# Kernel tuning notes

Hardware: AMD Instinct MI355X
Metric: run time of the kernel (lower is better)

Reference implementation:

```python
import jax, jax.numpy as jnp
import numpy as np

D_MODEL = 1024
N_HEADS = 16
D_HEAD = D_MODEL // N_HEADS
B, S = 4, 2048
NEG_INF = float('-inf')


def setup_inputs() -> dict:
    key = jax.random.key(0)
    ks = jax.random.split(key, 12)
    sc = 1.0 / np.sqrt(D_MODEL)
    inp = {
        'query': jax.random.normal(ks[0], (B, S, D_MODEL), jnp.float32),
        'key': jax.random.normal(ks[1], (B, S, D_MODEL), jnp.float32),
        'value': jax.random.normal(ks[2], (B, S, D_MODEL), jnp.float32),
        'mask': jnp.ones((B, S), jnp.int32),
        'W_q': jax.random.normal(ks[3], (D_MODEL, D_MODEL), jnp.float32) * sc,
        'b_q': jax.random.normal(ks[4], (D_MODEL,), jnp.float32) * sc,
        'W_k': jax.random.normal(ks[5], (D_MODEL, D_MODEL), jnp.float32) * sc,
        'b_k': jax.random.normal(ks[6], (D_MODEL,), jnp.float32) * sc,
        'W_v': jax.random.normal(ks[7], (D_MODEL, D_MODEL), jnp.float32) * sc,
        'b_v': jax.random.normal(ks[8], (D_MODEL,), jnp.float32) * sc,
        'W_o': jax.random.normal(ks[9], (D_MODEL, D_MODEL), jnp.float32) * sc,
        'b_o': jax.random.normal(ks[10], (D_MODEL,), jnp.float32) * sc,
    }
    return inp


def reference(query, key, value, mask, W_q, b_q, W_k, b_k, W_v, b_v, W_o, b_o):
    b, s, d = query.shape
    # QKV projections, split heads: [B,S,D] -> [B,H,S,Dh]
    def proj(x, W, bias):
        y = x @ W + bias
        return y.reshape(b, s, N_HEADS, D_HEAD).transpose(0, 2, 1, 3)
    q = proj(query, W_q, b_q)
    k = proj(key, W_k, b_k)
    v = proj(value, W_v, b_v)
    # NOTE: original scales by d_head**2 (not sqrt) — kept faithful.
    e = jnp.einsum('bhqd,bhkd->bhqk', q, k) / (D_HEAD ** 2)
    # key padding mask: [B,S] -> additive [B,1,1,S]
    pad = jnp.where(mask == 0, NEG_INF, 0.0).astype(e.dtype)[:, None, None, :]
    e = e + pad
    # causal mask: additive lower-triangular
    causal = jnp.where(jnp.tril(jnp.ones((s, s), bool)), 0.0, NEG_INF).astype(e.dtype)
    e = e + causal[None, None, :, :]
    a = jax.nn.softmax(e, axis=-1)
    c = jnp.einsum('bhqk,bhkd->bhqd', a, v)  # [B,H,S,Dh]
    c = c.transpose(0, 2, 1, 3).reshape(b, s, d)
    return c @ W_o + b_o
```

## Files before the change

### kernel.cpp

```cpp
#include <hip/hip_runtime.h>

typedef __bf16 bf16;
typedef unsigned int u32;
typedef float f32x4 __attribute__((ext_vector_type(4)));
typedef __bf16 bf16x4 __attribute__((ext_vector_type(4)));
typedef __bf16 bf16x8 __attribute__((ext_vector_type(8)));

#define MFMA(a, b, c) __builtin_amdgcn_mfma_f32_16x16x32_bf16((a), (b), (c), 0, 0, 0)

static constexpr int Bc = 4;
static constexpr int Sc = 2048;
static constexpr int Hc = 16;
static constexpr int DHc = 64;
static constexpr int Dc = 1024;
static constexpr int Mc = Bc * Sc;

__device__ __forceinline__ void load_lds16(const bf16* gp, bf16* lp) {
    __builtin_amdgcn_global_load_lds(
        reinterpret_cast<const __attribute__((address_space(1))) u32*>(
            reinterpret_cast<uintptr_t>(gp)),
        reinterpret_cast<__attribute__((address_space(3))) u32*>(
            static_cast<u32>(reinterpret_cast<uintptr_t>(lp))),
        16, 0, 0);
}

__global__ void fill_diag(float* out, int n) {
    int i = blockIdx.x * 256 + threadIdx.x;
    if (i < n) out[i] = 1000.0f;
}

__global__ __launch_bounds__(256) void cvt_bf16(const float* __restrict__ in,
                                                bf16* __restrict__ out, int n) {
    int i = (blockIdx.x * 256 + threadIdx.x) * 8;
    if (i < n) {
        f32x4 a = *(const f32x4*)&in[i];
        f32x4 b = *(const f32x4*)&in[i + 4];
        bf16x8 v;
#pragma unroll
        for (int j = 0; j < 4; ++j) { v[j] = (bf16)a[j]; v[j + 4] = (bf16)b[j]; }
        *(bf16x8*)&out[i] = v;
    }
}

__global__ __launch_bounds__(256) void transpose4(
    const float* __restrict__ A0, const float* __restrict__ A1,
    const float* __restrict__ A2, const float* __restrict__ A3,
    bf16* __restrict__ O0, bf16* __restrict__ O1,
    bf16* __restrict__ O2, bf16* __restrict__ O3) {
    __shared__ bf16 t[32][33];
    const float* in = blockIdx.z == 0 ? A0 : blockIdx.z == 1 ? A1
                    : blockIdx.z == 2 ? A2 : A3;
    bf16* out = blockIdx.z == 0 ? O0 : blockIdx.z == 1 ? O1
              : blockIdx.z == 2 ? O2 : O3;
    int x = blockIdx.x * 32 + threadIdx.x;
#pragma unroll
    for (int j = 0; j < 32; j += 8) {
        int y = blockIdx.y * 32 + threadIdx.y + j;
        t[threadIdx.y + j][threadIdx.x] = (bf16)in[y * 1024 + x];
    }
    __syncthreads();
    int x2 = blockIdx.y * 32 + threadIdx.x;
#pragma unroll
    for (int j = 0; j < 32; j += 8) {
        int y2 = blockIdx.x * 32 + threadIdx.y + j;
        out[y2 * 1024 + x2] = t[threadIdx.x][threadIdx.y + j];
    }
}

template <int MODE, typename TOUT>
__global__ __launch_bounds__(256) void gemm_bt(const bf16* __restrict__ A,
                                               const bf16* __restrict__ Wt,
                                               const float* __restrict__ bias,
                                               TOUT* __restrict__ out,
                                               int M, int N, int K) {
    __shared__ alignas(16) bf16 As[3][128 * 32];
    __shared__ alignas(16) bf16 Bs[3][128 * 32];
    const int tid = threadIdx.x;
    const int wave = tid >> 6, lane = tid & 63;
    const int quad = lane >> 4, l16 = lane & 15;
    const int wr = (wave >> 1) * 64, wc = (wave & 1) * 64;
    const int id = blockIdx.y * 8 + blockIdx.x;
    const int sw = (id & 7) * 64 + (id >> 3);
    const int row0 = (sw >> 3) * 128, col0 = (sw & 7) * 128;

    const int sr = wave * 32 + (lane >> 2);
    const int sk = (lane & 3) * 8;
    const bf16* gA = &A[(size_t)(row0 + sr) * K + sk];
    const bf16* gB = &Wt[(size_t)(col0 + sr) * K + sk];
    const int wo = wave * 32 * 32;

#define GSTAGE(BUF, KOFF)                                                   \
    do {                                                                    \
        load_lds16(gA + (KOFF), &As[BUF][wo]);                              \
        load_lds16(gA + (KOFF) + 16 * K, &As[BUF][wo + 16 * 32]);           \
        load_lds16(gB + (KOFF), &Bs[BUF][wo]);                              \
        load_lds16(gB + (KOFF) + 16 * K, &Bs[BUF][wo + 16 * 32]);           \
    } while (0)

    f32x4 acc[4][4];
#pragma unroll
    for (int mi = 0; mi < 4; ++mi)
#pragma unroll
        for (int ni = 0; ni < 4; ++ni)
            acc[mi][ni] = (f32x4){0.f, 0.f, 0.f, 0.f};

    const int nk = K / 32;
    GSTAGE(0, 0);
    GSTAGE(1, 32);
    asm volatile("s_waitcnt vmcnt(4)" ::: "memory");
    __builtin_amdgcn_s_barrier();
    __builtin_amdgcn_sched_barrier(0);

    int cur = 0, nxt = 2;
#pragma unroll 1
    for (int i = 0; i < nk; ++i) {
        if (i + 2 < nk) GSTAGE(nxt, (i + 2) * 32);

        bf16x8 af[4], bf_[4];
#pragma unroll
        for (int mi = 0; mi < 4; ++mi)
            af[mi] = *(const bf16x8*)&As[cur][(wr + mi * 16 + l16) * 32 + quad * 8];
#pragma unroll
        for (int ni = 0; ni < 4; ++ni)
            bf_[ni] = *(const bf16x8*)&Bs[cur][(wc + ni * 16 + l16) * 32 + quad * 8];
#pragma unroll
        for (int mi = 0; mi < 4; ++mi)
#pragma unroll
            for (int ni = 0; ni < 4; ++ni)
                acc[mi][ni] = MFMA(af[mi], bf_[ni], acc[mi][ni]);

        if (i + 2 < nk) asm volatile("s_waitcnt vmcnt(4)" ::: "memory");
        else            asm volatile("s_waitcnt vmcnt(0)" ::: "memory");
        __builtin_amdgcn_s_barrier();
        __builtin_amdgcn_sched_barrier(0);
        cur = (cur == 2) ? 0 : cur + 1;
        nxt = (nxt == 2) ? 0 : nxt + 1;
    }
#undef GSTAGE

#pragma unroll
    for (int mi = 0; mi < 4; ++mi) {
#pragma unroll
        for (int ni = 0; ni < 4; ++ni) {
            int col = col0 + wc + ni * 16 + l16;
            float bv = bias[col];
#pragma unroll
            for (int r = 0; r < 4; ++r) {
                int row = row0 + wr + mi * 16 + quad * 4 + r;
                float v = acc[mi][ni][r] + bv;
                size_t off;
                if (MODE == 0) {
                    off = (size_t)row * N + col;
                } else {
                    int b = row >> 11, s = row & (Sc - 1);
                    int h = col >> 6, dh = col & (DHc - 1);
                    if (MODE == 1)
                        off = (((size_t)(b * Hc + h) * Sc + s) << 6) + dh;
                    else
                        off = (((size_t)(b * Hc + h) * DHc + dh) << 11) + s;
                }
                out[off] = (TOUT)v;
            }
        }
    }
}

static constexpr int LPP = 72;
static constexpr float CEXP = 1.4426950408889634f / 4096.0f;

__global__ __launch_bounds__(256, 2) void attn_fwd(const bf16* __restrict__ Q,
                                                   const bf16* __restrict__ K,
                                                   const bf16* __restrict__ Vt,
                                                   const int* __restrict__ mask,
                                                   bf16* __restrict__ Ctx) {
    __shared__ alignas(16) bf16 Ks[2][64 * 64];
    __shared__ alignas(16) bf16 Vs[2][64 * 64];
    __shared__ alignas(16) bf16 Ps[4][32 * LPP];
    __shared__ alignas(16) float msk_all[Sc];

    const int tid = threadIdx.x;
    const int wave = tid >> 6, lane = tid & 63;
    const int quad = lane >> 4, l16 = lane & 15;
    const int id = blockIdx.y * 8 + blockIdx.x;
    const int sw = (id & 7) * 64 + (id >> 3);
    const int bh = sw >> 3, p = sw & 7;
    const int b = bh >> 4, h = bh & 15;

    {
        const int i = tid * 8;
        int4 m0 = *(const int4*)&mask[b * Sc + i];
        int4 m1 = *(const int4*)&mask[b * Sc + i + 4];
        f32x4 f0 = {m0.x ? 0.f : -1e30f, m0.y ? 0.f : -1e30f,
                    m0.z ? 0.f : -1e30f, m0.w ? 0.f : -1e30f};
        f32x4 f1 = {m1.x ? 0.f : -1e30f, m1.y ? 0.f : -1e30f,
                    m1.z ? 0.f : -1e30f, m1.w ? 0.f : -1e30f};
        *(f32x4*)&msk_all[i] = f0;
        *(f32x4*)&msk_all[i + 4] = f1;
    }

    const int swz = ((lane & 7) ^ (lane >> 3)) << 4;
    const int rA = wave * 16 + (lane >> 3);
    const char* gK0 = (const char*)K + (size_t)bh * Sc * (DHc * 2)
                    + (size_t)rA * 128 + swz;
    const char* gV0 = (const char*)Vt + (size_t)bh * DHc * (Sc * 2)
                    + (size_t)rA * (Sc * 2) + swz;
    bf16* lK0 = &Ks[0][(wave * 16) * 64];
    bf16* lV0 = &Vs[0][(wave * 16) * 64];

    const int m7 = l16 & 7;
    const int gsw0 = ((0 + quad) ^ m7) * 8;
    const int gsw1 = ((4 + quad) ^ m7) * 8;

#define STAGE(BUF, KB)                                                        \
    do {                                                                      \
        load_lds16((const bf16*)(gK0 + (size_t)(KB) * 128),                   \
                   lK0 + (BUF) * (64 * 64));                                  \
        load_lds16((const bf16*)(gK0 + (size_t)(KB) * 128 + 1024),            \
                   lK0 + (BUF) * (64 * 64) + 8 * 64);                         \
        load_lds16((const bf16*)(gV0 + (size_t)(KB) * 2),                     \
                   lV0 + (BUF) * (64 * 64));                                  \
        load_lds16((const bf16*)(gV0 + (size_t)(KB) * 2 + 8 * 4096),          \
                   lV0 + (BUF) * (64 * 64) + 8 * 64);                         \
    } while (0)

#pragma unroll 1
    for (int pass = 0; pass < 2; ++pass) {
        const int qt = pass ? p : 15 - p;
        const int qr0 = qt * 128 + wave * 32;
        const int qmax = qr0 + 31;

        bf16x8 bq[2][2];
#pragma unroll
        for (int mt = 0; mt < 2; ++mt) {
            const size_t qoff = ((size_t)bh * Sc + qr0 + mt * 16 + l16) * DHc;
            bq[mt][0] = *(const bf16x8*)&Q[qoff + quad * 8];
            bq[mt][1] = *(const bf16x8*)&Q[qoff + 32 + quad * 8];
        }

        f32x4 accO[2][4];
#pragma unroll
        for (int mt = 0; mt < 2; ++mt)
#pragma unroll
            for (int oi = 0; oi < 4; ++oi) accO[mt][oi] = (f32x4){0.f, 0.f, 0.f, 0.f};
        float l_part[2] = {0.f, 0.f};

        const int nkt = 2 * qt + 2;
        STAGE(0, 0);
        __syncthreads();
        int cur = 0;
#pragma unroll 1
        for (int kt = 0; kt < nkt; ++kt) {
            const int kb = kt * 64;
            if (kt + 1 < nkt) STAGE(cur ^ 1, kb + 64);
            if (kb <= qmax) {
                const bf16* Kb_ = &Ks[cur][0];
                const bf16* Vb_ = &Vs[cur][0];

                f32x4 st[2][4];
                __builtin_amdgcn_s_setprio(1);
#pragma unroll
                for (int kti = 0; kti < 4; ++kti) {
                    bf16x8 ak0 = *(const bf16x8*)&Kb_[(kti * 16 + l16) * 64 + gsw0];
                    bf16x8 ak1 = *(const bf16x8*)&Kb_[(kti * 16 + l16) * 64 + gsw1];
#pragma unroll
                    for (int mt = 0; mt < 2; ++mt) {
                        f32x4 z = {0.f, 0.f, 0.f, 0.f};
                        z = MFMA(ak0, bq[mt][0], z);
                        z = MFMA(ak1, bq[mt][1], z);
                        st[mt][kti] = z;
                    }
                }
                __builtin_amdgcn_s_setprio(0);

#define SM_TILE(DIAG)                                                          \
                _Pragma("unroll")                                              \
                for (int mt = 0; mt < 2; ++mt) {                               \
                    _Pragma("unroll")                                          \
                    for (int kti = 0; kti < 4; ++kti) {                        \
                        const f32x4 mkv =                                      \
                            *(const f32x4*)&msk_all[kb + kti * 16 + quad * 4]; \
                        const int cbase =                                      \
                            kb + kti * 16 + quad * 4 - (qr0 + mt * 16);        \
                        bf16x4 pv;                                             \
                        _Pragma("unroll")                                      \
                        for (int r = 0; r < 4; ++r) {                          \
                            float s = st[mt][kti][r] * CEXP + mkv[r];          \
                            if (DIAG) s = (cbase + r > l16) ? -1e30f : s;      \
                            float p_ = __builtin_amdgcn_exp2f(s);              \
                            l_part[mt] += p_;                                  \
                            pv[r] = (bf16)p_;                                  \
                        }                                                      \
                        *(bf16x4*)&Ps[wave][(mt * 16 + l16) * LPP +            \
                                            kti * 16 + quad * 4] = pv;         \
                    }                                                          \
                }
                if (kb + 63 > qr0) { SM_TILE(1) } else { SM_TILE(0) }
#undef SM_TILE

                __builtin_amdgcn_s_setprio(1);
#pragma unroll
                for (int kk = 0; kk < 2; ++kk) {
                    bf16x8 ap0 = *(const bf16x8*)&Ps[wave][(l16) * LPP + kk * 32 + quad * 8];
                    bf16x8 ap1 = *(const bf16x8*)&Ps[wave][(16 + l16) * LPP + kk * 32 + quad * 8];
                    const int vg = kk ? gsw1 : gsw0;
#pragma unroll
                    for (int oi = 0; oi < 4; ++oi) {
                        bf16x8 bv = *(const bf16x8*)&Vb_[(oi * 16 + l16) * 64 + vg];
                        accO[0][oi] = MFMA(ap0, bv, accO[0][oi]);
                        accO[1][oi] = MFMA(ap1, bv, accO[1][oi]);
                    }
                }
                __builtin_amdgcn_s_setprio(0);
            }
            asm volatile("s_waitcnt vmcnt(0)" ::: "memory");
            __builtin_amdgcn_s_barrier();
            __builtin_amdgcn_sched_barrier(0);
            cur ^= 1;
        }

        float lvi[2][4];
#pragma unroll
        for (int mt = 0; mt < 2; ++mt) {
            float l = l_part[mt];
            l += __shfl_xor(l, 16);
            l += __shfl_xor(l, 32);
#pragma unroll
            for (int r = 0; r < 4; ++r)
                lvi[mt][r] = __builtin_amdgcn_rcpf(__shfl(l, quad * 4 + r));
        }
#pragma unroll
        for (int mt = 0; mt < 2; ++mt)
#pragma unroll
            for (int oi = 0; oi < 4; ++oi)
#pragma unroll
                for (int r = 0; r < 4; ++r) {
                    int s = qr0 + mt * 16 + quad * 4 + r;
                    int dh = oi * 16 + l16;
                    float v = accO[mt][oi][r] * lvi[mt][r];
                    Ctx[((size_t)b * Sc + s) * Dc + h * DHc + dh] = (bf16)v;
                }
    }
#undef STAGE
}

extern "C" void kernel_launch(void* const* d_in, const int* in_sizes, int n_in,
                              void* d_out, int out_size, void* d_ws, size_t ws_size,
                              hipStream_t stream) {
    const float* query = (const float*)d_in[0];
    const float* key_i = (const float*)d_in[1];
    const float* value = (const float*)d_in[2];
    const int* mask    = (const int*)d_in[3];
    const float* W_q = (const float*)d_in[4];
    const float* b_q = (const float*)d_in[5];
    const float* W_k = (const float*)d_in[6];
    const float* b_k = (const float*)d_in[7];
    const float* W_v = (const float*)d_in[8];
    const float* b_v = (const float*)d_in[9];
    const float* W_o = (const float*)d_in[10];
    const float* b_o = (const float*)d_in[11];
    float* out = (float*)d_out;

    const size_t MB = 1024 * 1024;
    const size_t NEED = 72 * MB;
    if (ws_size < NEED) {
        fill_diag<<<(out_size + 255) / 256, 256, 0, stream>>>(out, out_size);
        return;
    }

    char* ws = (char*)d_ws;
    bf16* WtQ = (bf16*)(ws + 0 * MB);
    bf16* WtK = (bf16*)(ws + 2 * MB);
    bf16* WtV = (bf16*)(ws + 4 * MB);
    bf16* WtO = (bf16*)(ws + 6 * MB);
    bf16* Xin = (bf16*)(ws + 8 * MB);
    bf16* Ctx = (bf16*)(ws + 8 * MB);
    bf16* Qb  = (bf16*)(ws + 24 * MB);
    bf16* Kb  = (bf16*)(ws + 40 * MB);
    bf16* Vtb = (bf16*)(ws + 56 * MB);

    transpose4<<<dim3(32, 32, 4), dim3(32, 8), 0, stream>>>(
        W_q, W_k, W_v, W_o, WtQ, WtK, WtV, WtO);

    const int ncv = Mc * Dc;
    dim3 gg(Dc / 128, Mc / 128);

    cvt_bf16<<<ncv / (256 * 8), 256, 0, stream>>>(query, Xin, ncv);
    gemm_bt<1, bf16><<<gg, 256, 0, stream>>>(Xin, WtQ, b_q, Qb, Mc, Dc, Dc);
    cvt_bf16<<<ncv / (256 * 8), 256, 0, stream>>>(key_i, Xin, ncv);
    gemm_bt<1, bf16><<<gg, 256, 0, stream>>>(Xin, WtK, b_k, Kb, Mc, Dc, Dc);
    cvt_bf16<<<ncv / (256 * 8), 256, 0, stream>>>(value, Xin, ncv);
    gemm_bt<2, bf16><<<gg, 256, 0, stream>>>(Xin, WtV, b_v, Vtb, Mc, Dc, Dc);

    attn_fwd<<<dim3(8, Bc * Hc), 256, 0, stream>>>(Qb, Kb, Vtb, mask, Ctx);

    gemm_bt<0, float><<<gg, 256, 0, stream>>>(Ctx, WtO, b_o, out, Mc, Dc, Dc);
}
```

Measured before the change: 319.6 us.

## Fuse fp32-to-bf16 input conversion into a batched QKV projection GEMM

Removes the three separate cvt_bf16 passes and three projection GEMM launches. A single z-batched gemm_qkv kernel loads fp32 activations straight into LDS with a swizzled layout and converts them to bf16 in registers before the MFMA. This drops the write and re-read of the bf16 copy of each input and cuts the launch count. In exchange, the A tile in LDS is twice as large (fp32), the kernel uses double buffering with a full vmcnt(0) wait each iteration instead of the triple-buffered pipeline, and each fragment load pays extra conversion ALU work.

```diff
diff --git a/kernel.cpp b/kernel.cpp
--- a/kernel.cpp
+++ b/kernel.cpp
@@ -15,7 +15,7 @@
 static constexpr int Dc = 1024;
 static constexpr int Mc = Bc * Sc;
 
-__device__ __forceinline__ void load_lds16(const bf16* gp, bf16* lp) {
+__device__ __forceinline__ void load_lds16(const void* gp, void* lp) {
     __builtin_amdgcn_global_load_lds(
         reinterpret_cast<const __attribute__((address_space(1))) u32*>(
             reinterpret_cast<uintptr_t>(gp)),
@@ -27,19 +27,6 @@
 __global__ void fill_diag(float* out, int n) {
     int i = blockIdx.x * 256 + threadIdx.x;
     if (i < n) out[i] = 1000.0f;
-}
-
-__global__ __launch_bounds__(256) void cvt_bf16(const float* __restrict__ in,
-                                                bf16* __restrict__ out, int n) {
-    int i = (blockIdx.x * 256 + threadIdx.x) * 8;
-    if (i < n) {
-        f32x4 a = *(const f32x4*)&in[i];
-        f32x4 b = *(const f32x4*)&in[i + 4];
-        bf16x8 v;
-#pragma unroll
-        for (int j = 0; j < 4; ++j) { v[j] = (bf16)a[j]; v[j + 4] = (bf16)b[j]; }
-        *(bf16x8*)&out[i] = v;
-    }
 }
 
 __global__ __launch_bounds__(256) void transpose4(
@@ -67,11 +54,123 @@
     }
 }
 
-template <int MODE, typename TOUT>
+__global__ __launch_bounds__(256) void gemm_qkv(
+    const float* __restrict__ Aq, const float* __restrict__ Ak,
+    const float* __restrict__ Av,
+    const bf16* __restrict__ Wq, const bf16* __restrict__ Wk,
+    const bf16* __restrict__ Wv,
+    const float* __restrict__ bq, const float* __restrict__ bk,
+    const float* __restrict__ bv,
+    bf16* __restrict__ Oq, bf16* __restrict__ Ok, bf16* __restrict__ Ov) {
+    __shared__ alignas(16) float As[2][128 * 32];
+    __shared__ alignas(16) bf16 Bs[2][128 * 32];
+    const int z = blockIdx.z;
+    const float* A = z == 0 ? Aq : z == 1 ? Ak : Av;
+    const bf16* Wt = z == 0 ? Wq : z == 1 ? Wk : Wv;
+    const float* bias = z == 0 ? bq : z == 1 ? bk : bv;
+    bf16* out = z == 0 ? Oq : z == 1 ? Ok : Ov;
+    const bool vmode = (z == 2);
+
+    const int tid = threadIdx.x;
+    const int wave = tid >> 6, lane = tid & 63;
+    const int quad = lane >> 4, l16 = lane & 15;
+    const int m7 = l16 & 7;
+    const int wr = (wave >> 1) * 64, wc = (wave & 1) * 64;
+    const int id = blockIdx.y * 8 + blockIdx.x;
+    const int sw = (id & 7) * 64 + (id >> 3);
+    const int row0 = (sw >> 3) * 128, col0 = (sw & 7) * 128;
+
+    const int arow = wave * 32 + (lane >> 3);
+    const int agr = (lane & 7) ^ ((lane >> 3) & 7);
+    const float* gA = &A[(size_t)(row0 + arow) * Dc + agr * 4];
+    const int sr = wave * 32 + (lane >> 2);
+    const int sk = (lane & 3) * 8;
+    const bf16* gB = &Wt[(size_t)(col0 + sr) * Dc + sk];
+
+#define QSTAGE(BUF, KOFF)                                                    \
+    do {                                                                     \
+        load_lds16(gA + (KOFF),           &As[BUF][(wave * 32 + 0) * 32]);   \
+        load_lds16(gA + (KOFF) + 8 * Dc,  &As[BUF][(wave * 32 + 8) * 32]);   \
+        load_lds16(gA + (KOFF) + 16 * Dc, &As[BUF][(wave * 32 + 16) * 32]);  \
+        load_lds16(gA + (KOFF) + 24 * Dc, &As[BUF][(wave * 32 + 24) * 32]);  \
+        load_lds16(gB + (KOFF), &Bs[BUF][wave * 32 * 32]);                   \
+        load_lds16(gB + (KOFF) + 16 * Dc, &Bs[BUF][wave * 32 * 32 + 16 * 32]); \
+    } while (0)
+
+    f32x4 acc[4][4];
+#pragma unroll
+    for (int mi = 0; mi < 4; ++mi)
+#pragma unroll
+        for (int ni = 0; ni < 4; ++ni)
+            acc[mi][ni] = (f32x4){0.f, 0.f, 0.f, 0.f};
+
+    const int ga = (2 * quad) ^ m7, gb = ga ^ 1;
+
+    QSTAGE(0, 0);
+    asm volatile("s_waitcnt vmcnt(0)" ::: "memory");
+    __builtin_amdgcn_s_barrier();
+    __builtin_amdgcn_sched_barrier(0);
+
+    int cur = 0;
+#pragma unroll 1
+    for (int i = 0; i < Dc / 32; ++i) {
+        if (i + 1 < Dc / 32) QSTAGE(cur ^ 1, (i + 1) * 32);
+
+        bf16x8 af[4], bfr[4];
+#pragma unroll
+        for (int mi = 0; mi < 4; ++mi) {
+            const int row = wr + mi * 16 + l16;
+            f32x4 a0 = *(const f32x4*)&As[cur][row * 32 + ga * 4];
+            f32x4 a1 = *(const f32x4*)&As[cur][row * 32 + gb * 4];
+#pragma unroll
+            for (int j = 0; j < 4; ++j) {
+                af[mi][j] = (bf16)a0[j];
+                af[mi][j + 4] = (bf16)a1[j];
+            }
+        }
+#pragma unroll
+        for (int ni = 0; ni < 4; ++ni)
+            bfr[ni] = *(const bf16x8*)&Bs[cur][(wc + ni * 16 + l16) * 32 + quad * 8];
+#pragma unroll
+        for (int mi = 0; mi < 4; ++mi)
+#pragma unroll
+            for (int ni = 0; ni < 4; ++ni)
+                acc[mi][ni] = MFMA(af[mi], bfr[ni], acc[mi][ni]);
+
+        asm volatile("s_waitcnt vmcnt(0)" ::: "memory");
+        __builtin_amdgcn_s_barrier();
+        __builtin_amdgcn_sched_barrier(0);
+        cur ^= 1;
+    }
+#undef QSTAGE
+
+#pragma unroll
+    for (int mi = 0; mi < 4; ++mi) {
+#pragma unroll
+        for (int ni = 0; ni < 4; ++ni) {
+            int col = col0 + wc + ni * 16 + l16;
+            float bv = bias[col];
+#pragma unroll
+            for (int r = 0; r < 4; ++r) {
+                int row = row0 + wr + mi * 16 + quad * 4 + r;
+                float v = acc[mi][ni][r] + bv;
+                int b = row >> 11, s = row & (Sc - 1);
+                int h = col >> 6, dh = col & (DHc - 1);
+                size_t off;
+                if (!vmode)
+                    off = (((size_t)(b * Hc + h) * Sc + s) << 6) + dh;
+                else
+                    off = (((size_t)(b * Hc + h) * DHc + dh) << 11) + s;
+                out[off] = (bf16)v;
+            }
+        }
+    }
+}
+
 __global__ __launch_bounds__(256) void gemm_bt(const bf16* __restrict__ A,
                                                const bf16* __restrict__ Wt,
                                                const float* __restrict__ bias,
-                                               TOUT* __restrict__ out,
+                                               float* __restrict__ out,
                                                int M, int N, int K) {
     __shared__ alignas(16) bf16 As[3][128 * 32];
     __shared__ alignas(16) bf16 Bs[3][128 * 32];
@@ -147,19 +246,7 @@
 #pragma unroll
             for (int r = 0; r < 4; ++r) {
                 int row = row0 + wr + mi * 16 + quad * 4 + r;
-                float v = acc[mi][ni][r] + bv;
-                size_t off;
-                if (MODE == 0) {
-                    off = (size_t)row * N + col;
-                } else {
-                    int b = row >> 11, s = row & (Sc - 1);
-                    int h = col >> 6, dh = col & (DHc - 1);
-                    if (MODE == 1)
-                        off = (((size_t)(b * Hc + h) * Sc + s) << 6) + dh;
-                    else
-                        off = (((size_t)(b * Hc + h) * DHc + dh) << 11) + s;
-                }
-                out[off] = (TOUT)v;
+                out[(size_t)row * N + col] = acc[mi][ni][r] + bv;
             }
         }
     }
@@ -372,26 +459,18 @@
     bf16* WtK = (bf16*)(ws + 2 * MB);
     bf16* WtV = (bf16*)(ws + 4 * MB);
     bf16* WtO = (bf16*)(ws + 6 * MB);
-    bf16* Xin = (bf16*)(ws + 8 * MB);
-    bf16* Ctx = (bf16*)(ws + 8 * MB);
-    bf16* Qb  = (bf16*)(ws + 24 * MB);
-    bf16* Kb  = (bf16*)(ws + 40 * MB);
-    bf16* Vtb = (bf16*)(ws + 56 * MB);
+    bf16* Qb  = (bf16*)(ws + 8 * MB);
+    bf16* Kb  = (bf16*)(ws + 24 * MB);
+    bf16* Vtb = (bf16*)(ws + 40 * MB);
+    bf16* Ctx = (bf16*)(ws + 56 * MB);
 
     transpose4<<<dim3(32, 32, 4), dim3(32, 8), 0, stream>>>(
         W_q, W_k, W_v, W_o, WtQ, WtK, WtV, WtO);
 
-    const int ncv = Mc * Dc;
-    dim3 gg(Dc / 128, Mc / 128);
-
-    cvt_bf16<<<ncv / (256 * 8), 256, 0, stream>>>(query, Xin, ncv);
-    gemm_bt<1, bf16><<<gg, 256, 0, stream>>>(Xin, WtQ, b_q, Qb, Mc, Dc, Dc);
-    cvt_bf16<<<ncv / (256 * 8), 256, 0, stream>>>(key_i, Xin, ncv);
-    gemm_bt<1, bf16><<<gg, 256, 0, stream>>>(Xin, WtK, b_k, Kb, Mc, Dc, Dc);
-    cvt_bf16<<<ncv / (256 * 8), 256, 0, stream>>>(value, Xin, ncv);
-    gemm_bt<2, bf16><<<gg, 256, 0, stream>>>(Xin, WtV, b_v, Vtb, Mc, Dc, Dc);
+    gemm_qkv<<<dim3(8, 64, 3), 256, 0, stream>>>(
+        query, key_i, value, WtQ, WtK, WtV, b_q, b_k, b_v, Qb, Kb, Vtb);
 
     attn_fwd<<<dim3(8, Bc * Hc), 256, 0, stream>>>(Qb, Kb, Vtb, mask, Ctx);
 
-    gemm_bt<0, float><<<gg, 256, 0, stream>>>(Ctx, WtO, b_o, out, Mc, Dc, Dc);
-}
+    gemm_bt<<<dim3(8, 64), 256, 0, stream>>>(Ctx, WtO, b_o, out, Mc, Dc, Dc);
+}
```

After: 343.8 us. 7.6% more time.
